# Kernel tuning notes

Hardware: AMD Instinct MI355X
Metric: run time of the kernel (lower is better)

Reference implementation:

```python
import jax, jax.numpy as jnp
import numpy as np

DIM = 16777216


def spu(x):
    # SPU(x) = x^2 - 0.5 for x >= 0, sigmoid(-x) - 1 for x < 0
    return jnp.where(x >= 0, x * x - 0.5, jax.nn.sigmoid(-x) - 1.0)


def setup_inputs() -> dict:
    key = jax.random.key(0)
    k1, k2, k3 = jax.random.split(key, 3)
    center = jax.random.normal(k1, (1, DIM), dtype=jnp.float32)
    width = jnp.abs(jax.random.normal(k2, (1, DIM), dtype=jnp.float32))
    l_in = center - width
    u_in = center + width
    # x is a concrete point (heuristic 'x' uses it as the lower-bound tangent point;
    # it gets clipped to [l, u] inside the bound computation anyway)
    x = jax.random.normal(k3, (1, DIM), dtype=jnp.float32)
    return {"x": x, "l_in": l_in, "u_in": u_in}


def reference(x, l_in, u_in):
    # x_out = SPU applied elementwise (SPU().forward(x))
    x_out = spu(x)

    # _1D_box_bounds, vectorized, faithful to the original branch order:
    #   if l >= 0:   l' = spu(l); u' = spu(u)
    #   elif u <= 0: l' = spu(u); u' = spu(l')   (NB: original code reassigns l first,
    #                                             so u' = spu(spu(u)) -- reproduced faithfully)
    #   else:        u' = spu(u); l' = -0.5
    spu_l = spu(l_in)
    spu_u = spu(u_in)
    l_ge0 = l_in >= 0
    u_le0 = u_in <= 0

    l_out = jnp.where(l_ge0, spu_l, jnp.where(u_le0, spu_u, jnp.float32(-0.5)))
    u_out = jnp.where(l_ge0, spu_u, jnp.where(u_le0, spu(spu_u), spu_u))
    return (x_out, l_out, u_out)
```

## Files before the change

### kernel.cpp

```cpp
#include <hip/hip_runtime.h>

__device__ __forceinline__ float spu_f(float v) {
    if (v >= 0.f) {
        return fmaf(v, v, -0.5f);
    }
    float e = __expf(v);
    return -e / (1.f + e);
}

__global__ __launch_bounds__(256) void spu_layer_kernel(
    const float4* __restrict__ x,
    const float4* __restrict__ l,
    const float4* __restrict__ u,
    float4* __restrict__ xo,
    float4* __restrict__ lo,
    float4* __restrict__ uo,
    int n4)
{
    int i = blockIdx.x * blockDim.x + threadIdx.x;
    if (i >= n4) return;

    float4 xv = x[i];
    float4 lv = l[i];
    float4 uv = u[i];
    float4 xr, lr, ur;

    const float* xp = (const float*)&xv;
    const float* lp = (const float*)&lv;
    const float* up = (const float*)&uv;
    float* xq = (float*)&xr;
    float* lq = (float*)&lr;
    float* uq = (float*)&ur;

#pragma unroll
    for (int k = 0; k < 4; ++k) {
        float xk = xp[k], lk = lp[k], uk = up[k];

        float sl = spu_f(lk);
        float su = spu_f(uk);

        float l_out, u_out;
        if (lk >= 0.f) {
            l_out = sl;
            u_out = su;
        } else if (uk <= 0.f) {
            l_out = su;
            u_out = spu_f(su);
        } else {
            l_out = -0.5f;
            u_out = su;
        }

        xq[k] = spu_f(xk);
        lq[k] = l_out;
        uq[k] = u_out;
    }

    xo[i] = xr;
    lo[i] = lr;
    uo[i] = ur;
}

extern "C" void kernel_launch(void* const* d_in, const int* in_sizes, int n_in,
                              void* d_out, int out_size, void* d_ws, size_t ws_size,
                              hipStream_t stream) {
    const float* x = (const float*)d_in[0];
    const float* l = (const float*)d_in[1];
    const float* u = (const float*)d_in[2];
    float* out = (float*)d_out;

    const int n  = in_sizes[0];
    const int n4 = n / 4;

    float* xo = out;
    float* lo = out + n;
    float* uo = out + 2 * (size_t)n;

    dim3 block(256);
    dim3 grid((n4 + 255) / 256);
    spu_layer_kernel<<<grid, block, 0, stream>>>(
        (const float4*)x, (const float4*)l, (const float4*)u,
        (float4*)xo, (float4*)lo, (float4*)uo, n4);
}
```

Measured before the change: 333.9 us.

## Use nontemporal vector loads/stores, branchless SPU, and two float4 per thread

Loads and stores switch to nontemporal builtins on ext_vector float4, which is meant to keep streaming data from polluting the cache. The SPU function becomes branchless with a fast reciprocal, so exp and the select always run and the divergent branches go away. Each thread now handles two float4 chunks and the grid is halved. The trade is more ALU work per element in exchange for less control flow and fewer blocks, in a kernel that is memory bound.

```diff
diff --git a/kernel.cpp b/kernel.cpp
--- a/kernel.cpp
+++ b/kernel.cpp
@@ -1,64 +1,59 @@
 #include <hip/hip_runtime.h>
 
+typedef float vf4 __attribute__((ext_vector_type(4)));
+
 __device__ __forceinline__ float spu_f(float v) {
-    if (v >= 0.f) {
-        return fmaf(v, v, -0.5f);
+    float e   = __expf(v);
+    float neg = -e * __builtin_amdgcn_rcpf(1.f + e);
+    float pos = fmaf(v, v, -0.5f);
+    return v >= 0.f ? pos : neg;
+}
+
+__device__ __forceinline__ void process4(
+    const vf4* __restrict__ x, const vf4* __restrict__ l, const vf4* __restrict__ u,
+    vf4* __restrict__ xo, vf4* __restrict__ lo, vf4* __restrict__ uo, int i)
+{
+    vf4 xv = __builtin_nontemporal_load(x + i);
+    vf4 lv = __builtin_nontemporal_load(l + i);
+    vf4 uv = __builtin_nontemporal_load(u + i);
+    vf4 xr, lr, ur;
+
+#pragma unroll
+    for (int k = 0; k < 4; ++k) {
+        float xk = xv[k], lk = lv[k], uk = uv[k];
+
+        float sl  = spu_f(lk);
+        float su  = spu_f(uk);
+        float ssu = spu_f(su);
+
+        float l_out = lk >= 0.f ? sl : (uk <= 0.f ? su : -0.5f);
+        float u_out = (lk < 0.f && uk <= 0.f) ? ssu : su;
+
+        xr[k] = spu_f(xk);
+        lr[k] = l_out;
+        ur[k] = u_out;
     }
-    float e = __expf(v);
-    return -e / (1.f + e);
+
+    __builtin_nontemporal_store(xr, xo + i);
+    __builtin_nontemporal_store(lr, lo + i);
+    __builtin_nontemporal_store(ur, uo + i);
 }
 
 __global__ __launch_bounds__(256) void spu_layer_kernel(
-    const float4* __restrict__ x,
-    const float4* __restrict__ l,
-    const float4* __restrict__ u,
-    float4* __restrict__ xo,
-    float4* __restrict__ lo,
-    float4* __restrict__ uo,
+    const vf4* __restrict__ x,
+    const vf4* __restrict__ l,
+    const vf4* __restrict__ u,
+    vf4* __restrict__ xo,
+    vf4* __restrict__ lo,
+    vf4* __restrict__ uo,
     int n4)
 {
-    int i = blockIdx.x * blockDim.x + threadIdx.x;
-    if (i >= n4) return;
-
-    float4 xv = x[i];
-    float4 lv = l[i];
-    float4 uv = u[i];
-    float4 xr, lr, ur;
-
-    const float* xp = (const float*)&xv;
-    const float* lp = (const float*)&lv;
-    const float* up = (const float*)&uv;
-    float* xq = (float*)&xr;
-    float* lq = (float*)&lr;
-    float* uq = (float*)&ur;
-
-#pragma unroll
-    for (int k = 0; k < 4; ++k) {
-        float xk = xp[k], lk = lp[k], uk = up[k];
-
-        float sl = spu_f(lk);
-        float su = spu_f(uk);
-
-        float l_out, u_out;
-        if (lk >= 0.f) {
-            l_out = sl;
-            u_out = su;
-        } else if (uk <= 0.f) {
-            l_out = su;
-            u_out = spu_f(su);
-        } else {
-            l_out = -0.5f;
-            u_out = su;
-        }
-
-        xq[k] = spu_f(xk);
-        lq[k] = l_out;
-        uq[k] = u_out;
-    }
-
-    xo[i] = xr;
-    lo[i] = lr;
-    uo[i] = ur;
+    int base = blockIdx.x * (blockDim.x * 2) + threadIdx.x;
+    if (base < n4)
+        process4(x, l, u, xo, lo, uo, base);
+    int base2 = base + blockDim.x;
+    if (base2 < n4)
+        process4(x, l, u, xo, lo, uo, base2);
 }
 
 extern "C" void kernel_launch(void* const* d_in, const int* in_sizes, int n_in,
@@ -77,8 +72,8 @@
     float* uo = out + 2 * (size_t)n;
 
     dim3 block(256);
-    dim3 grid((n4 + 255) / 256);
+    dim3 grid((n4 + 511) / 512);
     spu_layer_kernel<<<grid, block, 0, stream>>>(
-        (const float4*)x, (const float4*)l, (const float4*)u,
-        (float4*)xo, (float4*)lo, (float4*)uo, n4);
+        (const vf4*)x, (const vf4*)l, (const vf4*)u,
+        (vf4*)xo, (vf4*)lo, (vf4*)uo, n4);
 }
```

Result: no change. 329.1 us (-1.4%).
